# Performance work log

Measured on AMD Instinct MI355X. Metric: run time of the kernel, lower is better.

The kernel has to match this reference:

```python
import jax, jax.numpy as jnp
import numpy as np
from jax import lax

VOCAB, MAX_LEN, EMB, H = 50000, 128, 300, 50
BATCH = 1024
BN_SCALE = 1.0 / np.sqrt(1.0 + 0.001)  # batch_normalization with mean=0, var=1, eps=1e-3


def setup_inputs() -> dict:
    key = jax.random.key(0)
    ks = jax.random.split(key, 10)
    return {
        "x1": jax.random.randint(ks[0], (BATCH, MAX_LEN), 0, VOCAB, dtype=jnp.int32),
        "x2": jax.random.randint(ks[1], (BATCH, MAX_LEN), 0, VOCAB, dtype=jnp.int32),
        "embedding_matrix": jax.random.normal(ks[2], (VOCAB, EMB), jnp.float32),
        "W_fw": jax.random.normal(ks[3], (EMB + H, 4 * H), jnp.float32) * 0.05,
        "b_fw": jnp.zeros((4 * H,), jnp.float32),
        "W_bw": jax.random.normal(ks[4], (EMB + H, 4 * H), jnp.float32) * 0.05,
        "b_bw": jnp.zeros((4 * H,), jnp.float32),
        "W1": jax.random.normal(ks[5], (2 * H, 25), jnp.float32) * 0.1,
        "b1": jax.random.normal(ks[6], (25,), jnp.float32) * 0.1,
        "W2": jax.random.normal(ks[7], (25, 3), jnp.float32) * 0.1,
        "b2": jax.random.normal(ks[8], (3,), jnp.float32) * 0.1,
    }


def _lstm_scan(xs, W, b):
    # xs: [T, B, E]; BasicLSTMCell: gates = [x, h] @ W + b, split i, j, f, o; forget_bias=1.0
    T, B, _ = xs.shape
    def step(carry, x):
        c, h = carry
        g = jnp.concatenate([x, h], axis=-1) @ W + b
        i, j, f, o = jnp.split(g, 4, axis=-1)
        c2 = c * jax.nn.sigmoid(f + 1.0) + jax.nn.sigmoid(i) * jnp.tanh(j)
        h2 = jnp.tanh(c2) * jax.nn.sigmoid(o)
        return (c2, h2), h2
    init = (jnp.zeros((B, H), xs.dtype), jnp.zeros((B, H), xs.dtype))
    _, hs = lax.scan(step, init, xs)
    return hs  # [T, B, H]


def reference(x1, x2, embedding_matrix, W_fw, b_fw, W_bw, b_bw, W1, b1, W2, b2):
    tokens = jnp.concatenate([x1, x2], axis=1)            # [B, 2*max_len]
    emb = embedding_matrix[tokens]                         # [B, T, E]
    xs = jnp.transpose(emb, (1, 0, 2))                     # [T, B, E]
    h_fw = _lstm_scan(xs, W_fw, b_fw)                      # [T, B, H]
    h_bw = _lstm_scan(xs[::-1], W_bw, b_bw)                # [T, B, H] (time reversed)
    # static_bidirectional_rnn reverses bw outputs, so outputs[-1] pairs
    # fw at step T-1 with bw's first step (which consumed x_{T-1}).
    feat = jnp.concatenate([h_fw[-1], h_bw[0]], axis=-1)   # [B, 2H]
    bn = feat * BN_SCALE
    h1 = jax.nn.relu(bn @ W1 + b1)                         # dropout omitted (eval mode)
    out = h1 @ W2 + b2
    return out * BN_SCALE
```

## Files before the change

### kernel.cpp

```cpp
#include <hip/hip_runtime.h>
#include <hip/hip_bf16.h>


#define VOCAB 50000
#define EMB   300
#define HID   50
#define GATES 200
#define BATCH 1024
#define TT    256
#define NPAD  208
#define KPAD  320
#define BN_SCALE 0.9995003746877732f

typedef short bf16x8 __attribute__((ext_vector_type(8)));
typedef float f32x4  __attribute__((ext_vector_type(4)));

__device__ __forceinline__ float sigm(float x) {
    return 1.0f / (1.0f + __expf(-x));
}
__device__ __forceinline__ float tanh_f(float x) {
    return 1.0f - 2.0f / (__expf(2.0f * x) + 1.0f);
}
__device__ __forceinline__ unsigned short f32_to_bf16(float x) {
    unsigned int u = __float_as_uint(x);
    u += 0x7fffu + ((u >> 16) & 1u);
    return (unsigned short)(u >> 16);
}
__device__ __forceinline__ float bf16_to_f32(unsigned short h) {
    return __uint_as_float(((unsigned int)h) << 16);
}

__global__ __launch_bounds__(256) void split_w(const float* __restrict__ Wfw,
                                               unsigned short* __restrict__ WhT,
                                               unsigned short* __restrict__ WlT) {
    const int idx = blockIdx.x * 256 + threadIdx.x;
    if (idx >= NPAD * KPAD) return;
    const int n = idx / KPAD;
    const int k = idx - n * KPAD;
    float v = (n < GATES && k < EMB) ? Wfw[k * GATES + n] : 0.0f;
    const unsigned short hb = f32_to_bf16(v);
    const unsigned short lb = f32_to_bf16(v - bf16_to_f32(hb));
    WhT[idx] = hb;
    WlT[idx] = lb;
}

__global__ __launch_bounds__(256) void vocab_proj_mfma(const float* __restrict__ E,
                                                       const unsigned short* __restrict__ WhT,
                                                       const unsigned short* __restrict__ WlT,
                                                       float* __restrict__ P) {
    const int w  = threadIdx.x >> 6;
    const int l  = threadIdx.x & 63;
    const int lr = l & 15;
    const int lg = l >> 4;

    const int row    = blockIdx.x * 64 + w * 16 + lr;
    const int rclamp = (row < VOCAB) ? row : (VOCAB - 1);
    const float* Erow = E + (size_t)rclamp * EMB;

    f32x4 acc[13];
#pragma unroll
    for (int f = 0; f < 13; ++f) acc[f] = (f32x4){0.f, 0.f, 0.f, 0.f};

    for (int ks = 0; ks < 10; ++ks) {
        const int k0 = ks * 32 + lg * 8;
        float av[8];
        if (ks < 9) {
            const float4 a0 = *reinterpret_cast<const float4*>(Erow + k0);
            const float4 a1 = *reinterpret_cast<const float4*>(Erow + k0 + 4);
            av[0] = a0.x; av[1] = a0.y; av[2] = a0.z; av[3] = a0.w;
            av[4] = a1.x; av[5] = a1.y; av[6] = a1.z; av[7] = a1.w;
        } else {
#pragma unroll
            for (int j = 0; j < 8; ++j) {
                const int kk = k0 + j;
                av[j] = (kk < EMB) ? Erow[kk] : 0.0f;
            }
        }
        bf16x8 ah, al;
#pragma unroll
        for (int j = 0; j < 8; ++j) {
            const unsigned short hb = f32_to_bf16(av[j]);
            ah[j] = (short)hb;
            al[j] = (short)f32_to_bf16(av[j] - bf16_to_f32(hb));
        }

#pragma unroll
        for (int f = 0; f < 13; ++f) {
            const int n = f * 16 + lr;
            const size_t boff = (size_t)n * KPAD + k0;
            const bf16x8 bh = *reinterpret_cast<const bf16x8*>(WhT + boff);
            const bf16x8 bl = *reinterpret_cast<const bf16x8*>(WlT + boff);
            acc[f] = __builtin_amdgcn_mfma_f32_16x16x32_bf16(ah, bh, acc[f], 0, 0, 0);
            acc[f] = __builtin_amdgcn_mfma_f32_16x16x32_bf16(al, bh, acc[f], 0, 0, 0);
            acc[f] = __builtin_amdgcn_mfma_f32_16x16x32_bf16(ah, bl, acc[f], 0, 0, 0);
        }
    }

    const int orow0 = blockIdx.x * 64 + w * 16 + lg * 4;
#pragma unroll
    for (int f = 0; f < 13; ++f) {
        const int col = f * 16 + lr;
        if (col < GATES) {
#pragma unroll
            for (int r = 0; r < 4; ++r) {
                const int orow = orow0 + r;
                if (orow < VOCAB) P[(size_t)orow * GATES + col] = acc[f][r];
            }
        }
    }
}

__global__ __launch_bounds__(128) void lstm_fw(const int* __restrict__ x1,
                                               const int* __restrict__ x2,
                                               const float* __restrict__ P,
                                               const float* __restrict__ Wfw,
                                               const float* __restrict__ bfw,
                                               float* __restrict__ feat) {
    const int b = blockIdx.x;
    const int w = threadIdx.x >> 6;
    const int l = threadIdx.x & 63;
    const int u = (l < HID) ? l : (HID - 1);
    const bool act_lane = (l < HID);

    __shared__ int   stok[TT];
    __shared__ float ex[2][2][HID][2];

    stok[threadIdx.x]       = x1[b * 128 + threadIdx.x];
    stok[128 + threadIdx.x] = x2[b * 128 + threadIdx.x];

    const int cA = u + (w ? 100 : 0);
    const int cB = u + (w ? 150 : 50);
    float wA[HID], wB[HID];
#pragma unroll
    for (int k = 0; k < HID; ++k) {
        const float* rowp = Wfw + (size_t)(EMB + k) * GATES;
        wA[k] = rowp[cA];
        wB[k] = rowp[cB];
    }
    float bA = bfw[cA] + (w ? 1.0f : 0.0f);
    float bB = bfw[cB];

    float c = 0.0f, h = 0.0f;
    __syncthreads();

    int tok = stok[0];
    float pA = P[(size_t)tok * GATES + cA];
    float pB = P[(size_t)tok * GATES + cB];
    int tokn = stok[1];

    for (int t = 0; t < TT; ++t) {
        float aA = pA + bA;
        float aB = pB + bB;

        {
            const float* pr = P + (size_t)tokn * GATES;
            pA = pr[cA];
            pB = pr[cB];
        }
        const int t2 = (t + 2 < TT) ? (t + 2) : (TT - 1);
        tokn = stok[t2];

#pragma unroll
        for (int k = 0; k < HID; ++k) {
            const float hk = __uint_as_float(
                __builtin_amdgcn_readlane(__float_as_uint(h), k));
            aA = fmaf(wA[k], hk, aA);
            aB = fmaf(wB[k], hk, aB);
        }

        const float e0 = sigm(aA);
        const float e1 = (w == 0) ? tanh_f(aB) : sigm(aB);
        if (act_lane)
            *reinterpret_cast<float2*>(&ex[t & 1][w][l][0]) = make_float2(e0, e1);

        asm volatile("s_waitcnt lgkmcnt(0)" ::: "memory");
        __builtin_amdgcn_s_barrier();

        const float2 o01 = *reinterpret_cast<const float2*>(&ex[t & 1][w ^ 1][u][0]);
        const float si = (w == 0) ? e0 : o01.x;
        const float tj = (w == 0) ? e1 : o01.y;
        const float sf = (w == 0) ? o01.x : e0;
        const float so = (w == 0) ? o01.y : e1;

        c = c * sf + si * tj;
        h = tanh_f(c) * so;
    }

    if (w == 0 && act_lane) feat[b * (2 * HID) + l] = h;
}

__global__ __launch_bounds__(256) void bw_mlp(const int* __restrict__ x2,
                                              const float* __restrict__ E,
                                              const float* __restrict__ Wbw,
                                              const float* __restrict__ bbw,
                                              const float* __restrict__ W1,
                                              const float* __restrict__ b1,
                                              const float* __restrict__ W2,
                                              const float* __restrict__ b2,
                                              const float* __restrict__ featfw,
                                              float* __restrict__ out) {
    const int b = blockIdx.x;
    const int t = threadIdx.x;

    __shared__ __align__(16) float sx[EMB + 4];
    __shared__ float sf[2 * HID];
    __shared__ float sg[GATES];
    __shared__ float sh1[25];

    const int tok = x2[b * 128 + 127];
    for (int e = t; e < EMB; e += 256) sx[e] = E[(size_t)tok * EMB + e];
    if (t < HID) sf[t] = featfw[b * (2 * HID) + t];
    __syncthreads();

    if (t < GATES) {
        float g0 = bbw[t], g1 = 0.0f, g2 = 0.0f, g3 = 0.0f;
        for (int e = 0; e < EMB; e += 4) {
            g0 = fmaf(sx[e + 0], Wbw[(e + 0) * GATES + t], g0);
            g1 = fmaf(sx[e + 1], Wbw[(e + 1) * GATES + t], g1);
            g2 = fmaf(sx[e + 2], Wbw[(e + 2) * GATES + t], g2);
            g3 = fmaf(sx[e + 3], Wbw[(e + 3) * GATES + t], g3);
        }
        sg[t] = (g0 + g1) + (g2 + g3);
    }
    __syncthreads();

    if (t < HID) {
        const float c2 = sigm(sg[t]) * tanh_f(sg[t + HID]);
        sf[HID + t] = tanh_f(c2) * sigm(sg[t + 3 * HID]);
    }
    __syncthreads();

    if (t < 25) {
        float a = 0.0f;
#pragma unroll 4
        for (int k = 0; k < 2 * HID; ++k)
            a = fmaf(sf[k], W1[k * 25 + t], a);
        a = fmaf(a, BN_SCALE, b1[t]);
        sh1[t] = fmaxf(a, 0.0f);
    }
    __syncthreads();

    if (t < 3) {
        float a = b2[t];
#pragma unroll
        for (int k = 0; k < 25; ++k)
            a = fmaf(sh1[k], W2[k * 3 + t], a);
        out[b * 3 + t] = a * BN_SCALE;
    }
}

extern "C" void kernel_launch(void* const* d_in, const int* in_sizes, int n_in,
                              void* d_out, int out_size, void* d_ws, size_t ws_size,
                              hipStream_t stream) {
    const int*   x1  = (const int*)d_in[0];
    const int*   x2  = (const int*)d_in[1];
    const float* E   = (const float*)d_in[2];
    const float* Wfw = (const float*)d_in[3];
    const float* bfw = (const float*)d_in[4];
    const float* Wbw = (const float*)d_in[5];
    const float* bbw = (const float*)d_in[6];
    const float* W1  = (const float*)d_in[7];
    const float* b1  = (const float*)d_in[8];
    const float* W2  = (const float*)d_in[9];
    const float* b2  = (const float*)d_in[10];
    float* out = (float*)d_out;

    float* Pm   = (float*)d_ws;
    float* feat = Pm + (size_t)VOCAB * GATES;
    unsigned short* WhT = (unsigned short*)(feat + BATCH * 2 * HID);
    unsigned short* WlT = WhT + (size_t)NPAD * KPAD;

    split_w<<<(NPAD * KPAD + 255) / 256, 256, 0, stream>>>(Wfw, WhT, WlT);
    vocab_proj_mfma<<<(VOCAB + 63) / 64, 256, 0, stream>>>(E, WhT, WlT, Pm);
    lstm_fw<<<BATCH, 128, 0, stream>>>(x1, x2, Pm, Wfw, bfw, feat);
    bw_mlp<<<BATCH, 256, 0, stream>>>(x2, E, Wbw, bbw, W1, b1, W2, b2, feat, out);
}
```

Before: 470.3 us.

## Split LSTM recurrence by hidden-k halves across waves instead of gate pairs

The forward LSTM kernel now has each of the two waves compute partial dot products for all four gates over half of the hidden inputs (25 each), exchange float4 partial sums through LDS, and then both waves apply every activation redundantly. Previously each wave computed full 50-term sums for two gates and exchanged activated values. The per-step serial FMA chain drops from 50 to 25, which shortens the critical path, at the cost of four activations per lane per step instead of two and wider LDS traffic. Launch bounds now request one block per SM, letting the compiler use more registers.

```diff
diff --git a/kernel.cpp b/kernel.cpp
--- a/kernel.cpp
+++ b/kernel.cpp
@@ -110,80 +110,77 @@
     }
 }
 
-__global__ __launch_bounds__(128) void lstm_fw(const int* __restrict__ x1,
-                                               const int* __restrict__ x2,
-                                               const float* __restrict__ P,
-                                               const float* __restrict__ Wfw,
-                                               const float* __restrict__ bfw,
-                                               float* __restrict__ feat) {
+__global__ __launch_bounds__(128, 1) void lstm_fw(const int* __restrict__ x1,
+                                                  const int* __restrict__ x2,
+                                                  const float* __restrict__ P,
+                                                  const float* __restrict__ Wfw,
+                                                  const float* __restrict__ bfw,
+                                                  float* __restrict__ feat) {
     const int b = blockIdx.x;
     const int w = threadIdx.x >> 6;
     const int l = threadIdx.x & 63;
     const int u = (l < HID) ? l : (HID - 1);
     const bool act_lane = (l < HID);
 
-    __shared__ int   stok[TT];
-    __shared__ float ex[2][2][HID][2];
+    __shared__ int    stok[TT];
+    __shared__ float4 ex[2][2][HID];
 
     stok[threadIdx.x]       = x1[b * 128 + threadIdx.x];
     stok[128 + threadIdx.x] = x2[b * 128 + threadIdx.x];
 
-    const int cA = u + (w ? 100 : 0);
-    const int cB = u + (w ? 150 : 50);
-    float wA[HID], wB[HID];
-#pragma unroll
-    for (int k = 0; k < HID; ++k) {
-        const float* rowp = Wfw + (size_t)(EMB + k) * GATES;
-        wA[k] = rowp[cA];
-        wB[k] = rowp[cB];
-    }
-    float bA = bfw[cA] + (w ? 1.0f : 0.0f);
-    float bB = bfw[cB];
+    float wi[25], wj[25], wf[25], wo[25];
+#pragma unroll
+    for (int k = 0; k < 25; ++k) {
+        const float* rowp = Wfw + (size_t)(EMB + 25 * w + k) * GATES;
+        wi[k] = rowp[u];
+        wj[k] = rowp[u + 50];
+        wf[k] = rowp[u + 100];
+        wo[k] = rowp[u + 150];
+    }
+    const float bi0 = bfw[u];
+    const float bj0 = bfw[u + 50];
+    const float bf0 = bfw[u + 100] + 1.0f;
+    const float bo0 = bfw[u + 150];
 
     float c = 0.0f, h = 0.0f;
     __syncthreads();
 
     int tok = stok[0];
-    float pA = P[(size_t)tok * GATES + cA];
-    float pB = P[(size_t)tok * GATES + cB];
+    const float* pr0 = P + (size_t)tok * GATES + u;
+    float pi = pr0[0], pj = pr0[50], pf = pr0[100], po = pr0[150];
     int tokn = stok[1];
 
     for (int t = 0; t < TT; ++t) {
-        float aA = pA + bA;
-        float aB = pB + bB;
-
+        const float cpi = pi, cpj = pj, cpf = pf, cpo = po;
         {
-            const float* pr = P + (size_t)tokn * GATES;
-            pA = pr[cA];
-            pB = pr[cB];
-        }
-        const int t2 = (t + 2 < TT) ? (t + 2) : (TT - 1);
-        tokn = stok[t2];
-
-#pragma unroll
-        for (int k = 0; k < HID; ++k) {
+            const float* pn = P + (size_t)tokn * GATES + u;
+            pi = pn[0]; pj = pn[50]; pf = pn[100]; po = pn[150];
+        }
+        tokn = stok[(t + 2 < TT) ? (t + 2) : (TT - 1)];
+
+        float gi = 0.0f, gj = 0.0f, gf = 0.0f, go = 0.0f;
+#pragma unroll
+        for (int k = 0; k < 25; ++k) {
             const float hk = __uint_as_float(
-                __builtin_amdgcn_readlane(__float_as_uint(h), k));
-            aA = fmaf(wA[k], hk, aA);
-            aB = fmaf(wB[k], hk, aB);
-        }
-
-        const float e0 = sigm(aA);
-        const float e1 = (w == 0) ? tanh_f(aB) : sigm(aB);
-        if (act_lane)
-            *reinterpret_cast<float2*>(&ex[t & 1][w][l][0]) = make_float2(e0, e1);
-
+                __builtin_amdgcn_readlane(__float_as_uint(h), 25 * w + k));
+            gi = fmaf(wi[k], hk, gi);
+            gj = fmaf(wj[k], hk, gj);
+            gf = fmaf(wf[k], hk, gf);
+            go = fmaf(wo[k], hk, go);
+        }
+
+        if (act_lane) ex[t & 1][w][l] = make_float4(gi, gj, gf, go);
         asm volatile("s_waitcnt lgkmcnt(0)" ::: "memory");
         __builtin_amdgcn_s_barrier();
-
-        const float2 o01 = *reinterpret_cast<const float2*>(&ex[t & 1][w ^ 1][u][0]);
-        const float si = (w == 0) ? e0 : o01.x;
-        const float tj = (w == 0) ? e1 : o01.y;
-        const float sf = (w == 0) ? o01.x : e0;
-        const float so = (w == 0) ? o01.y : e1;
-
-        c = c * sf + si * tj;
-        h = tanh_f(c) * so;
+        const float4 op = ex[t & 1][w ^ 1][u];
+
+        const float ai = gi + op.x + cpi + bi0;
+        const float aj = gj + op.y + cpj + bj0;
+        const float af = gf + op.z + cpf + bf0;
+        const float ao = go + op.w + cpo + bo0;
+
+        c = c * sigm(af) + sigm(ai) * tanh_f(aj);
+        h = tanh_f(c) * sigm(ao);
     }
 
     if (w == 0 && act_lane) feat[b * (2 * HID) + l] = h;
```

New measurement: 498.6 us. 6.0% more time.
